# Optimization experiments

Measured on AMD Instinct MI355X. Metric: run time of the kernel, lower is better.

The kernel has to match this reference:

```python
import jax, jax.numpy as jnp
import numpy as np

B, S, D, H, NS = 4, 2048, 1024, 16, 300
DK = D // H                      # 64
NSP = (NS + H - 1) // H * H      # 304 (padded skills)
DG = NSP // H                    # 19
NEG_FILL = -1e9                  # fp32 path in the torch module


def setup_inputs() -> dict:
    key = jax.random.key(0)
    ks = jax.random.split(key, 12)
    sc = 0.02
    return {
        "context_sequence": jax.random.normal(ks[0], (B, S, D), jnp.float32),
        "value_sequence": jax.random.normal(ks[1], (B, S, NS), jnp.float32),
        "mask": jnp.triu(jnp.ones((S, S), jnp.bool_), k=1),  # causal: True = masked
        # weights stored as [in, out] (math-equivalent to torch's x @ W.T + b)
        "Wq": jax.random.normal(ks[2], (D, D), jnp.float32) * sc,
        "bq": jnp.zeros((D,), jnp.float32),
        "Wk": jax.random.normal(ks[3], (D, D), jnp.float32) * sc,
        "bk": jnp.zeros((D,), jnp.float32),
        "Wv": jax.random.normal(ks[4], (NS, NS), jnp.float32) * sc,
        "bv": jnp.zeros((NS,), jnp.float32),
        "Wg": jax.random.normal(ks[5], (NS, D), jnp.float32) * sc,  # gain_to_context
        "bg": jnp.zeros((D,), jnp.float32),
        "Wo": jax.random.normal(ks[6], (D, D), jnp.float32) * sc,   # output_proj
        "bo": jnp.zeros((D,), jnp.float32),
    }


def reference(context_sequence, value_sequence, mask,
              Wq, bq, Wk, bk, Wv, bv, Wg, bg, Wo, bo):
    b = context_sequence.shape[0]
    orig_dtype = context_sequence.dtype

    # Q, K: [b, H, S, DK]
    Q = (context_sequence @ Wq + bq).reshape(b, -1, H, DK).transpose(0, 2, 1, 3)
    K = (context_sequence @ Wk + bk).reshape(b, -1, H, DK).transpose(0, 2, 1, 3)

    # intrinsic-gain V: project in skill space, zero-pad to NSP, split heads -> [b, H, S, DG]
    V_proj = value_sequence @ Wv + bv
    V_proj = jnp.pad(V_proj, ((0, 0), (0, 0), (0, NSP - NS)))
    V = V_proj.reshape(b, -1, H, DG).transpose(0, 2, 1, 3)

    # fp32 score upcast, scale by sqrt(d_k), mask, cast back, softmax
    scores = jnp.einsum('bhqd,bhkd->bhqk',
                        Q.astype(jnp.float32), K.astype(jnp.float32)) / np.sqrt(DK)
    scores = jnp.where(mask, NEG_FILL, scores).astype(orig_dtype)
    attn = jax.nn.softmax(scores, axis=-1)

    # [b, H, S, DG] -> [b, S, NSP] -> slice to NS
    head_gains = jnp.einsum('bhqk,bhkd->bhqd', attn, V)
    agg = head_gains.transpose(0, 2, 1, 3).reshape(b, -1, NSP)[..., :NS]

    output = agg @ Wg + bg            # gain_to_context
    return output @ Wo + bo           # output_proj (dropout is identity in eval)
```

## Files before the change

kernel.cpp:

```cpp
#include <hip/hip_runtime.h>
#include <hip/hip_bf16.h>

#define MROWS 8192
#define DMODEL 1024
#define SLEN 2048
#define NHEADS 16
#define DKH 64
#define DGH 19
#define NSKILL 300
#define KGPAD 320
#define AGG_LD 320
#define QK_LD 2048
#define VK 320
#define VTN 384

typedef __attribute__((ext_vector_type(8))) short short8;
typedef __attribute__((ext_vector_type(4))) float floatx4;

__device__ __forceinline__ float bf2f(unsigned short u) {
  union { unsigned int i; float f; } cv;
  cv.i = ((unsigned int)u) << 16;
  return cv.f;
}
__device__ __forceinline__ unsigned short f2bf(float f) {
  __hip_bfloat16 h = __float2bfloat16(f);
  unsigned short u;
  __builtin_memcpy(&u, &h, 2);
  return u;
}

__device__ __forceinline__ float exp2hw(float x) {
#if __has_builtin(__builtin_amdgcn_exp2f)
  return __builtin_amdgcn_exp2f(x);
#else
  return __expf(x * 0.6931471805599453f);
#endif
}
__device__ __forceinline__ unsigned int cvt_pk_bf16(float lo, float hi) {
  unsigned int r;
  asm("v_cvt_pk_bf16_f32 %0, %1, %2" : "=v"(r) : "v"(lo), "v"(hi));
  return r;
}

__device__ __forceinline__ void ld8(const float* p, float* v) {
  float4 a = *(const float4*)p;
  float4 b = *((const float4*)p + 1);
  v[0]=a.x; v[1]=a.y; v[2]=a.z; v[3]=a.w;
  v[4]=b.x; v[5]=b.y; v[6]=b.z; v[7]=b.w;
}
__device__ __forceinline__ void st1(float* p, float v) { *p = v; }
__device__ __forceinline__ void st1(__hip_bfloat16* p, float v) {
  unsigned short raw = f2bf(v); __builtin_memcpy(p, &raw, 2);
}
__device__ __forceinline__ void st8(__hip_bfloat16* p, const float* v) {
  ushort4 a, b;
  a.x=f2bf(v[0]); a.y=f2bf(v[1]); a.z=f2bf(v[2]); a.w=f2bf(v[3]);
  b.x=f2bf(v[4]); b.y=f2bf(v[5]); b.z=f2bf(v[6]); b.w=f2bf(v[7]);
  *(ushort4*)p = a;
  *((ushort4*)p + 1) = b;
}

__device__ __forceinline__ void gl_lds16(const void* g, void* l) {
  __builtin_amdgcn_global_load_lds(
      (const __attribute__((address_space(1))) unsigned int*)g,
      (__attribute__((address_space(3))) unsigned int*)l, 16, 0, 0);
}

__global__ __launch_bounds__(256)
void prep_mega_kernel(const float* __restrict__ X,
                      const float* __restrict__ Vin,
                      const float* __restrict__ Wg,
                      const float* __restrict__ bq, const float* __restrict__ bk,
                      const float* __restrict__ bv,
                      const float* __restrict__ Wq, const float* __restrict__ Wk,
                      const float* __restrict__ Wo, const float* __restrict__ Wv,
                      __hip_bfloat16* __restrict__ Xb,
                      __hip_bfloat16* __restrict__ Vb16,
                      __hip_bfloat16* __restrict__ Wgb,
                      float* __restrict__ biasqk, float* __restrict__ biasv,
                      float* __restrict__ z384,
                      __hip_bfloat16* __restrict__ Wtqk,
                      __hip_bfloat16* __restrict__ WoT,
                      __hip_bfloat16* __restrict__ Wvt)
{
  const int bid = blockIdx.x;
  const int t = threadIdx.x;
  if (bid < 8192) {
    int i = (bid * 256 + t) * 4;
    float4 v = *(const float4*)(X + i);
    ushort4 s;
    s.x = f2bf(v.x); s.y = f2bf(v.y); s.z = f2bf(v.z); s.w = f2bf(v.w);
    *(ushort4*)((__hip_bfloat16*)Xb + i) = s;
    return;
  }
  if (bid < 9472) {
    int idx = (bid - 8192) * 256 + t;
    int row = idx / 40;
    int c8  = (idx - row * 40) * 8;
    const float* ip = Vin + (size_t)row * NSKILL + c8;
    float v[8];
    if (c8 + 8 <= NSKILL) {
      ld8(ip, v);
    } else {
      #pragma unroll
      for (int u = 0; u < 8; u++)
        v[u] = (c8 + u < NSKILL) ? ip[u] : 0.f;
    }
    st8(Vb16 + (size_t)row * VK + c8, v);
    return;
  }
  if (bid < 9856) {
    int i4 = ((bid - 9472) * 256 + t) * 4;
    int r = i4 >> 10;
    ushort4 s = {0, 0, 0, 0};
    if (r < NSKILL) {
      float4 v = *(const float4*)(Wg + i4);
      s.x = f2bf(v.x); s.y = f2bf(v.y); s.z = f2bf(v.z); s.w = f2bf(v.w);
    }
    *(ushort4*)((__hip_bfloat16*)Wgb + i4) = s;
    return;
  }
  if (bid == 9856) {
    for (int i = t; i < 1024; i += 256) { biasqk[i] = bq[i]; biasqk[1024 + i] = bk[i]; }
    for (int i = t; i < 384; i += 256) {
      biasv[i] = (i < NSKILL) ? bv[i] : 0.f;
      z384[i] = 0.f;
    }
    return;
  }
  const float* W; __hip_bfloat16* Wt; int K, Nld, Ntrue, Kpad, kx, ny;
  if (bid < 10881)      { int l = bid - 9857;  W=Wq; Wt=Wtqk;            K=1024; Nld=1024; Ntrue=1024; Kpad=1024; kx=l&31; ny=l>>5; }
  else if (bid < 11905) { int l = bid - 10881; W=Wk; Wt=Wtqk+1024*1024;  K=1024; Nld=1024; Ntrue=1024; Kpad=1024; kx=l&31; ny=l>>5; }
  else if (bid < 12929) { int l = bid - 11905; W=Wo; Wt=WoT;             K=1024; Nld=1024; Ntrue=1024; Kpad=1024; kx=l&31; ny=l>>5; }
  else                  { int l = bid - 12929; W=Wv; Wt=Wvt;             K=NSKILL; Nld=NSKILL; Ntrue=NSKILL; Kpad=VK; kx=l%10; ny=l/10; }
  __shared__ float tb[32][33];
  const int k0 = kx * 32;
  const int n0 = ny * 32;
  const int tx = t & 31, ty = t >> 5;
  #pragma unroll
  for (int i = 0; i < 4; i++) {
    int k = k0 + ty + i*8;
    int nn = n0 + tx;
    tb[ty + i*8][tx] = (k < K && nn < Ntrue) ? W[(size_t)k * Nld + nn] : 0.f;
  }
  __syncthreads();
  #pragma unroll
  for (int i = 0; i < 4; i++) {
    int nn = n0 + ty + i*8;
    int kk = k0 + tx;
    st1(Wt + (size_t)nn * Kpad + kk, tb[tx][ty + i*8]);
  }
}

__device__ __forceinline__ void gemm_core(const short* __restrict__ Ag,
                                          const short* __restrict__ Bg,
                                          int lda, int ldb, int K,
                                          int m0, int n0,
                                          short* Al, short* Bl,
                                          int tid, floatx4 (&acc)[4][4])
{
  const int lane = tid & 63;
  const int wave = tid >> 6;
  const int wy = wave >> 1, wx = wave & 1;
  const int n = lane & 15;
  const int quad = lane >> 4;

  for (int k0 = 0; k0 < K; k0 += 64) {
    #pragma unroll
    for (int it = 0; it < 4; it++) {
      int ci = it*256 + tid;
      int r = ci >> 3, c = ci & 7;
      int cs = c ^ (r & 7);
      gl_lds16(Ag + (size_t)(m0 + r) * lda + k0 + cs*8, &Al[ci*8]);
    }
    #pragma unroll
    for (int it = 0; it < 4; it++) {
      int ci = it*256 + tid;
      int r = ci >> 3, c = ci & 7;
      int cs = c ^ (r & 7);
      gl_lds16(Bg + (size_t)(n0 + r) * ldb + k0 + cs*8, &Bl[ci*8]);
    }
    __syncthreads();

    #pragma unroll
    for (int s = 0; s < 2; s++) {
      short8 af[4], bfr[4];
      const int c = s*4 + quad;
      #pragma unroll
      for (int i = 0; i < 4; i++) {
        int r = wy*64 + i*16 + n;
        af[i] = *(const short8*)&Al[(r*8 + (c ^ (r & 7)))*8];
      }
      #pragma unroll
      for (int j = 0; j < 4; j++) {
        int r = wx*64 + j*16 + n;
        bfr[j] = *(const short8*)&Bl[(r*8 + (c ^ (r & 7)))*8];
      }
      #pragma unroll
      for (int i = 0; i < 4; i++)
        #pragma unroll
        for (int j = 0; j < 4; j++)
          acc[i][j] = __builtin_amdgcn_mfma_f32_16x16x32_bf16(af[i], bfr[j], acc[i][j], 0, 0, 0);
    }
    __syncthreads();
  }
}

__global__ __launch_bounds__(256)
void gemm_qk_vt_kernel(const __hip_bfloat16* __restrict__ Xb,
                       const __hip_bfloat16* __restrict__ Wtqk,
                       const float* __restrict__ biasqk,
                       __hip_bfloat16* __restrict__ QKbuf,
                       const __hip_bfloat16* __restrict__ Vb16,
                       const __hip_bfloat16* __restrict__ Wvt,
                       const float* __restrict__ biasv,
                       __hip_bfloat16* __restrict__ VT)
{
  __shared__ __align__(16) short Al[128*64];
  __shared__ __align__(16) short Bl[128*64];
  const int tid = threadIdx.x;
  const int lane = tid & 63;
  const int wave = tid >> 6;
  const int wy = wave >> 1, wx = wave & 1;
  const int n = lane & 15;
  const int quad = lane >> 4;

  floatx4 acc[4][4];
  #pragma unroll
  for (int i = 0; i < 4; i++)
    #pragma unroll
    for (int j = 0; j < 4; j++) acc[i][j] = (floatx4){0.f,0.f,0.f,0.f};

  if (blockIdx.x < 1024) {
    const int bx = blockIdx.x & 15, by = blockIdx.x >> 4;
    const int m0 = by * 128, n0 = bx * 128;
    gemm_core((const short*)Xb, (const short*)Wtqk, DMODEL, DMODEL, DMODEL,
              m0, n0, Al, Bl, tid, acc);
    float bj[4];
    #pragma unroll
    for (int j = 0; j < 4; j++) bj[j] = biasqk[n0 + wx*64 + j*16 + n];
    #pragma unroll
    for (int i = 0; i < 4; i++) {
      #pragma unroll
      for (int r = 0; r < 4; r++) {
        int row = m0 + wy*64 + i*16 + quad*4 + r;
        __hip_bfloat16* cp = QKbuf + (size_t)row * QK_LD;
        #pragma unroll
        for (int j = 0; j < 4; j++) {
          int col = n0 + wx*64 + j*16 + n;
          st1(cp + col, acc[i][j][r] + bj[j]);
        }
      }
    }
  } else {
    const int l = blockIdx.x - 1024;
    const int bx = l % 3, by = l / 3;
    const int m0 = by * 128, n0 = bx * 128;
    gemm_core((const short*)Vb16, (const short*)Wvt, VK, VK, VK,
              m0, n0, Al, Bl, tid, acc);
    float bj[4];
    #pragma unroll
    for (int j = 0; j < 4; j++) bj[j] = biasv[n0 + wx*64 + j*16 + n];
    #pragma unroll
    for (int i = 0; i < 4; i++) {
      int row0 = m0 + wy*64 + i*16 + quad*4;
      int bb = row0 >> 11, rin = row0 & 2047;
      #pragma unroll
      for (int j = 0; j < 4; j++) {
        int col = n0 + wx*64 + j*16 + n;
        ushort4 pk;
        pk.x = f2bf(acc[i][j][0] + bj[j]);
        pk.y = f2bf(acc[i][j][1] + bj[j]);
        pk.z = f2bf(acc[i][j][2] + bj[j]);
        pk.w = f2bf(acc[i][j][3] + bj[j]);
        *(ushort4*)(VT + ((size_t)bb * VTN + col) * SLEN + rin) = pk;
      }
    }
  }
}

__global__ __launch_bounds__(256)
void wgo_bgo_kernel(const __hip_bfloat16* __restrict__ WoT,
                    const __hip_bfloat16* __restrict__ Wgb,
                    const float* __restrict__ z384,
                    __hip_bfloat16* __restrict__ WgoT,
                    const float* __restrict__ bg, const float* __restrict__ Wo,
                    const float* __restrict__ bo, float* __restrict__ bgo)
{
  __shared__ __align__(16) short Al[128*64];
  __shared__ __align__(16) short Bl[128*64];
  const int tid = threadIdx.x;
  if (blockIdx.x < 24) {
    const int lane = tid & 63;
    const int wave = tid >> 6;
    const int wy = wave >> 1, wx = wave & 1;
    const int n = lane & 15;
    const int quad = lane >> 4;
    const int bx = blockIdx.x % 3, by = blockIdx.x / 3;
    const int m0 = by * 128, n0 = bx * 128;
    floatx4 acc[4][4];
    #pragma unroll
    for (int i = 0; i < 4; i++)
      #pragma unroll
      for (int j = 0; j < 4; j++) acc[i][j] = (floatx4){0.f,0.f,0.f,0.f};
    gemm_core((const short*)WoT, (const short*)Wgb, DMODEL, DMODEL, DMODEL,
              m0, n0, Al, Bl, tid, acc);
    float bj[4];
    #pragma unroll
    for (int j = 0; j < 4; j++) bj[j] = z384[n0 + wx*64 + j*16 + n];
    #pragma unroll
    for (int i = 0; i < 4; i++) {
      #pragma unroll
      for (int r = 0; r < 4; r++) {
        int row = m0 + wy*64 + i*16 + quad*4 + r;
        __hip_bfloat16* cp = WgoT + (size_t)row * 384;
        #pragma unroll
        for (int j = 0; j < 4; j++) {
          int col = n0 + wx*64 + j*16 + n;
          st1(cp + col, acc[i][j][r] + bj[j]);
        }
      }
    }
  } else {
    __shared__ float red[256];
    const int c   = tid & 15;
    const int jg  = tid >> 4;
    const int col = (blockIdx.x - 24) * 16 + c;
    float acc = 0.f;
    const int j0 = jg * 64;
    #pragma unroll 8
    for (int j = j0; j < j0 + 64; j++)
      acc = fmaf(bg[j], Wo[(size_t)j * DMODEL + col], acc);
    red[tid] = acc;
    __syncthreads();
    if (jg == 0) {
      float s = 0.f;
      #pragma unroll
      for (int g = 0; g < 16; g++) s += red[g*16 + c];
      bgo[col] = s + bo[col];
    }
  }
}

__global__ __launch_bounds__(256)
void gemm_final_kernel(const __hip_bfloat16* __restrict__ A,
                       const __hip_bfloat16* __restrict__ Bt,
                       const float* __restrict__ bias,
                       float* __restrict__ C)
{
  __shared__ __align__(16) short Al[128*64];
  __shared__ __align__(16) short Bl[128*64];
  const int tid = threadIdx.x;
  const int lane = tid & 63;
  const int wave = tid >> 6;
  const int wy = wave >> 1, wx = wave & 1;
  const int n = lane & 15;
  const int quad = lane >> 4;
  const int m0 = blockIdx.y * 128;
  const int n0 = blockIdx.x * 128;
  floatx4 acc[4][4];
  #pragma unroll
  for (int i = 0; i < 4; i++)
    #pragma unroll
    for (int j = 0; j < 4; j++) acc[i][j] = (floatx4){0.f,0.f,0.f,0.f};
  gemm_core((const short*)A, (const short*)Bt, KGPAD, 384, KGPAD,
            m0, n0, Al, Bl, tid, acc);
  float bj[4];
  #pragma unroll
  for (int j = 0; j < 4; j++) bj[j] = bias[n0 + wx*64 + j*16 + n];
  #pragma unroll
  for (int i = 0; i < 4; i++) {
    #pragma unroll
    for (int r = 0; r < 4; r++) {
      int row = m0 + wy*64 + i*16 + quad*4 + r;
      float* cp = C + (size_t)row * DMODEL;
      #pragma unroll
      for (int j = 0; j < 4; j++) {
        int col = n0 + wx*64 + j*16 + n;
        cp[col] = acc[i][j][r] + bj[j];
      }
    }
  }
}

#define ATT_BM 128
#define ATT_BK 64
#define ATT_GRID (24*64)

__global__ __launch_bounds__(256)
void attn_mfma_kernel(const __hip_bfloat16* __restrict__ Qb,
                      const __hip_bfloat16* __restrict__ Kb,
                      const __hip_bfloat16* __restrict__ VTg,
                      __hip_bfloat16* __restrict__ Agg,
                      float* __restrict__ Pl,
                      float* __restrict__ Po)
{
  __shared__ __align__(16) short Kf[2][64*64];
  __shared__ __align__(16) short Vf[2][32*64];
  __shared__ __align__(16) unsigned int Plds[4][2][4][16][4];

  const int tid  = threadIdx.x;
  const int lane = tid & 63;
  const int wave = tid >> 6;
  const int n    = lane & 15;
  const int quad = lane >> 4;

  const int cid = blockIdx.x >> 6;
  const int bh  = blockIdx.x & 63;
  const int h   = bh & 15;
  const int b   = bh >> 4;
  int qt, kt0, nt, mode;
  if (cid == 0)      { qt = 7;       kt0 = 0;  nt = 16; mode = 0; }
  else if (cid <= 8) { qt = cid + 7; kt0 = 0;  nt = 16; mode = 1; }
  else if (cid == 9) { qt = 15;      kt0 = 16; nt = 16; mode = 2; }
  else {
    int e = (cid - 10) >> 1;
    if (((cid - 10) & 1) == 0) { qt = 6 - e;  kt0 = 0;  nt = 14 - 2*e; mode = 0; }
    else                       { qt = 14 - e; kt0 = 16; nt = 14 - 2*e; mode = 2; }
  }
  const int qbase = qt * ATT_BM;
  const size_t bS = (size_t)b * SLEN;

  const float QSCALE = 0.18033688f;
  short8 qf[2][2];
  #pragma unroll
  for (int rf = 0; rf < 2; rf++)
    #pragma unroll
    for (int ks = 0; ks < 2; ks++) {
      const __hip_bfloat16* qp = Qb + (bS + qbase + wave*32 + rf*16 + n) * QK_LD
                                    + h*DKH + ks*32 + quad*8;
      short8 v = *(const short8*)qp;
      #pragma unroll
      for (int e = 0; e < 8; e++) {
        float f = bf2f((unsigned short)v[e]) * QSCALE;
        v[e] = (short)f2bf(f);
      }
      qf[rf][ks] = v;
    }

  const short* kp;
  {
    int f = tid;
    int nn = f & 15, q = (f >> 4) & 3, c = (f >> 6) & 3;
    kp = (const short*)Kb + (bS + kt0*64 + c*16 + nn) * QK_LD + h*DKH + q*8;
  }
  const short* vp;
  {
    int g = tid;
    int vn = g & 15, vq = (g >> 4) & 3, sv = (g >> 6) & 1, cv = g >> 7;
    vp = (const short*)VTg + ((size_t)b * VTN + h*DGH + cv*16 + vn) * SLEN
         + kt0*64 + sv*32 + vq*8;
  }

  floatx4 of[2][2];
  float lrow[2];
  #pragma unroll
  for (int rf = 0; rf < 2; rf++) {
    #pragma unroll
    for (int cv = 0; cv < 2; cv++) of[rf][cv] = (floatx4){0.f,0.f,0.f,0.f};
    lrow[rf] = 0.f;
  }

  const int wrow_max = qbase + wave*32 + 31;

  auto stage = [&](int buf) {
    gl_lds16(kp,      &Kf[buf][tid*8]);
    gl_lds16(kp + 32, &Kf[buf][(tid + 256)*8]);
    gl_lds16(vp,      &Vf[buf][tid*8]);
    kp += 64 * QK_LD;
    vp += 64;
  };

  auto compute_tile = [&](int buf, int kbase) {
    if (kbase > wrow_max) return;
    #pragma unroll
    for (int rf = 0; rf < 2; rf++) {
      floatx4 sf[4];
      __builtin_amdgcn_s_setprio(1);
      #pragma unroll
      for (int cf = 0; cf < 4; cf++) {
        short8 k0v = *(const short8*)&Kf[buf][((0*4 + cf)*64 + lane)*8];
        short8 k1v = *(const short8*)&Kf[buf][((1*4 + cf)*64 + lane)*8];
        floatx4 a2 = (floatx4){0.f,0.f,0.f,0.f};
        a2 = __builtin_amdgcn_mfma_f32_16x16x32_bf16(k0v, qf[rf][0], a2, 0, 0, 0);
        a2 = __builtin_amdgcn_mfma_f32_16x16x32_bf16(k1v, qf[rf][1], a2, 0, 0, 0);
        sf[cf] = a2;
      }
      __builtin_amdgcn_s_setprio(0);

      const int qrow = qbase + wave*32 + rf*16 + n;
      if (kbase + 63 > qbase + wave*32 + rf*16) {
        #pragma unroll
        for (int cf = 0; cf < 4; cf++)
          #pragma unroll
          for (int r = 0; r < 4; r++) {
            int key = kbase + cf*16 + quad*4 + r;
            if (key > qrow) sf[cf][r] = -INFINITY;
          }
      }
      float rs = 0.f;
      #pragma unroll
      for (int cf = 0; cf < 4; cf++)
        #pragma unroll
        for (int r = 0; r < 4; r++) {
          float p = exp2hw(sf[cf][r]);
          sf[cf][r] = p;
          rs += p;
        }
      lrow[rf] += rs;

      #pragma unroll
      for (int cf = 0; cf < 4; cf++) {
        unsigned int w0 = cvt_pk_bf16(sf[cf][0], sf[cf][1]);
        unsigned int w1 = cvt_pk_bf16(sf[cf][2], sf[cf][3]);
        int s   = cf >> 1;
        int qt2 = 2*(cf & 1) + (quad >> 1);
        int jp  = 2*(quad & 1);
        *(uint2*)&Plds[wave][s][qt2][n][jp] = make_uint2(w0, w1);
      }
      short8 p0 = *(const short8*)&Plds[wave][0][quad][n][0];
      short8 p1 = *(const short8*)&Plds[wave][1][quad][n][0];
      __builtin_amdgcn_s_setprio(1);
      #pragma unroll
      for (int cv = 0; cv < 2; cv++) {
        short8 v0 = *(const short8*)&Vf[buf][((cv*2 + 0)*64 + lane)*8];
        short8 v1 = *(const short8*)&Vf[buf][((cv*2 + 1)*64 + lane)*8];
        floatx4 a2 = of[rf][cv];
        a2 = __builtin_amdgcn_mfma_f32_16x16x32_bf16(v0, p0, a2, 0, 0, 0);
        a2 = __builtin_amdgcn_mfma_f32_16x16x32_bf16(v1, p1, a2, 0, 0, 0);
        of[rf][cv] = a2;
      }
      __builtin_amdgcn_s_setprio(0);
    }
  };

  stage(0);
  for (int kt = 0; kt < nt; kt += 2) {
    stage(1);
    asm volatile("s_waitcnt vmcnt(3)" ::: "memory");
    __builtin_amdgcn_s_barrier();
    __builtin_amdgcn_sched_barrier(0);
    compute_tile(0, (kt0 + kt) * ATT_BK);
    __builtin_amdgcn_sched_barrier(0);
    __builtin_amdgcn_s_barrier();

    if (kt + 2 < nt) {
      stage(0);
      asm volatile("s_waitcnt vmcnt(3)" ::: "memory");
    } else {
      asm volatile("s_waitcnt vmcnt(0)" ::: "memory");
    }
    __builtin_amdgcn_s_barrier();
    __builtin_amdgcn_sched_barrier(0);
    compute_tile(1, (kt0 + kt + 1) * ATT_BK);
    __builtin_amdgcn_sched_barrier(0);
    __builtin_amdgcn_s_barrier();
  }

  #pragma unroll
  for (int rf = 0; rf < 2; rf++) {
    lrow[rf] += __shfl_xor(lrow[rf], 16);
    lrow[rf] += __shfl_xor(lrow[rf], 32);
  }

  if (mode == 0) {
    #pragma unroll
    for (int rf = 0; rf < 2; rf++) {
      float inv = 1.f / lrow[rf];
      int row = qbase + wave*32 + rf*16 + n;
      __hip_bfloat16* op = Agg + (bS + row)*AGG_LD + h*DGH;
      #pragma unroll
      for (int cv = 0; cv < 2; cv++)
        #pragma unroll
        for (int r = 0; r < 4; r++) {
          int dim = cv*16 + quad*4 + r;
          if (dim < DGH) st1(op + dim, of[rf][cv][r] * inv);
        }
    }
    if (h == 15) {
      int row = qbase + (tid >> 1);
      int c0 = 304 + (tid & 1) * 8;
      float z[8] = {0.f,0.f,0.f,0.f,0.f,0.f,0.f,0.f};
      st8(Agg + (bS + row)*AGG_LD + c0, z);
    }
  } else {
    const int p = (qt - 8) * 64 + bh;
    const int sl = mode - 1;
    #pragma unroll
    for (int rf = 0; rf < 2; rf++) {
      int rowl = wave*32 + rf*16 + n;
      size_t ri = (size_t)(sl*512 + p)*128 + rowl;
      float* po = Po + ri*20;
      #pragma unroll
      for (int cv = 0; cv < 2; cv++)
        #pragma unroll
        for (int r = 0; r < 4; r++) {
          int dim = cv*16 + quad*4 + r;
          if (dim < DGH) po[dim] = of[rf][cv][r];
        }
      if (quad == 0) Pl[ri] = lrow[rf];
    }
  }
}

__global__ __launch_bounds__(256)
void attn_combine_kernel(const float* __restrict__ Pl,
                         const float* __restrict__ Po,
                         __hip_bfloat16* __restrict__ Agg)
{
  int idx = blockIdx.x * 256 + threadIdx.x;
  int p = idx >> 7, rowl = idx & 127;
  int qt = 8 + (p >> 6), bh = p & 63, h = bh & 15, b = bh >> 4;
  size_t riA = (size_t)p*128 + rowl;
  size_t riB = (size_t)(512 + p)*128 + rowl;
  float inv = 1.f / (Pl[riA] + Pl[riB]);
  const float* oA = Po + riA*20;
  const float* oB = Po + riB*20;
  size_t row = (size_t)b*SLEN + qt*128 + rowl;
  __hip_bfloat16* op = Agg + row*AGG_LD + h*DGH;
  #pragma unroll
  for (int d = 0; d < DGH; d++)
    st1(op + d, (oA[d] + oB[d]) * inv);
  if (h == 15) {
    uint4 z = {0,0,0,0};
    *(uint4*)(Agg + row*AGG_LD + 304) = z;
    *(uint4*)(Agg + row*AGG_LD + 312) = z;
  }
}

extern "C" void kernel_launch(void* const* d_in, const int* in_sizes, int n_in,
                              void* d_out, int out_size, void* d_ws, size_t ws_size,
                              hipStream_t stream) {
  const float* X   = (const float*)d_in[0];
  const float* Vin = (const float*)d_in[1];
  const float* Wq  = (const float*)d_in[3];
  const float* bq  = (const float*)d_in[4];
  const float* Wk  = (const float*)d_in[5];
  const float* bk  = (const float*)d_in[6];
  const float* Wv  = (const float*)d_in[7];
  const float* bv  = (const float*)d_in[8];
  const float* Wg  = (const float*)d_in[9];
  const float* bg  = (const float*)d_in[10];
  const float* Wo  = (const float*)d_in[11];
  const float* bo  = (const float*)d_in[12];
  float* out = (float*)d_out;

  char* ws = (char*)d_ws;
  __hip_bfloat16* Xb    = (__hip_bfloat16*)(ws);
  __hip_bfloat16* AggB  = (__hip_bfloat16*)(ws);
  __hip_bfloat16* WgoT  = (__hip_bfloat16*)(ws + 12582912);
  float*          bgoW  = (float*)         (ws + 13369344);
  __hip_bfloat16* QKbuf = (__hip_bfloat16*)(ws + 16777216);
  __hip_bfloat16* WoT   = (__hip_bfloat16*)(ws + 50331648);

  char* ob = (char*)d_out;
  __hip_bfloat16* Wtqk   = (__hip_bfloat16*)(ob);
  float*          biasqk = (float*)(ob + 4194304);
  __hip_bfloat16* Vb16   = (__hip_bfloat16*)(ob + 4202496);
  float*          biasv  = (float*)(ob + 9445376);
  float*          z384   = (float*)(ob + 9446912);
  __hip_bfloat16* Wgb    = (__hip_bfloat16*)(ob + 9448448);
  __hip_bfloat16* Wvt    = (__hip_bfloat16*)(ob + 10234880);
  float*          Pl     = (float*)(ob + 524288);
  float*          Po     = (float*)(ob + 1048576);
  __hip_bfloat16* VT     = (__hip_bfloat16*)(ob + 12582912);

  dim3 blk(256);
  prep_mega_kernel<<<dim3(13049), blk, 0, stream>>>(
      X, Vin, Wg, bq, bk, bv, Wq, Wk, Wo, Wv,
      Xb, Vb16, Wgb, biasqk, biasv, z384, Wtqk, WoT, Wvt);

  gemm_qk_vt_kernel<<<dim3(1216), blk, 0, stream>>>(
      Xb, Wtqk, biasqk, QKbuf, Vb16, Wvt, biasv, VT);

  wgo_bgo_kernel<<<dim3(88), blk, 0, stream>>>(
      WoT, Wgb, z384, WgoT, bg, Wo, bo, bgoW);

  attn_mfma_kernel<<<dim3(ATT_GRID), dim3(256), 0, stream>>>(
      QKbuf, QKbuf + 1024, VT, AggB, Pl, Po);

  attn_combine_kernel<<<dim3(256), blk, 0, stream>>>(Pl, Po, AggB);

  gemm_final_kernel<<<dim3(8, 64), blk, 0, stream>>>(AggB, WgoT, bgoW, out);
}
```

Before: 267.3 us.

## Merge weight-fold kernel into prep and QK GEMM launches; simplify attention staging

Removes the separate wgo_bgo kernel launch. The bias-fold dot product moves into extra blocks of the prep kernel, and the Wo·Wg fold GEMM moves into extra blocks of the QK/VT GEMM kernel, saving one launch and its tail. Separately, the attention loop drops its double-buffered prefetch with vmcnt waits and raw barriers. It now loads both 64-key tiles at once, then uses __syncthreads before and after computing them. That simplifies synchronization but loses the overlap of global-to-LDS loads with MFMA compute, which could slow the attention kernel.

```diff
diff --git a/kernel.cpp b/kernel.cpp
--- a/kernel.cpp
+++ b/kernel.cpp
@@ -74,6 +74,7 @@
                       const float* __restrict__ bv,
                       const float* __restrict__ Wq, const float* __restrict__ Wk,
                       const float* __restrict__ Wo, const float* __restrict__ Wv,
+                      const float* __restrict__ bg, const float* __restrict__ bo,
                       __hip_bfloat16* __restrict__ Xb,
                       __hip_bfloat16* __restrict__ Vb16,
                       __hip_bfloat16* __restrict__ Wgb,
@@ -81,7 +82,8 @@
                       float* __restrict__ z384,
                       __hip_bfloat16* __restrict__ Wtqk,
                       __hip_bfloat16* __restrict__ WoT,
-                      __hip_bfloat16* __restrict__ Wvt)
+                      __hip_bfloat16* __restrict__ Wvt,
+                      float* __restrict__ bgo)
 {
   const int bid = blockIdx.x;
   const int t = threadIdx.x;
@@ -125,6 +127,26 @@
     for (int i = t; i < 384; i += 256) {
       biasv[i] = (i < NSKILL) ? bv[i] : 0.f;
       z384[i] = 0.f;
+    }
+    return;
+  }
+  if (bid >= 13049) {
+    __shared__ float red[256];
+    const int c   = t & 15;
+    const int jg  = t >> 4;
+    const int col = (bid - 13049) * 16 + c;
+    float acc = 0.f;
+    const int j0 = jg * 64;
+    #pragma unroll 8
+    for (int j = j0; j < j0 + 64; j++)
+      acc = fmaf(bg[j], Wo[(size_t)j * DMODEL + col], acc);
+    red[t] = acc;
+    __syncthreads();
+    if (jg == 0) {
+      float s = 0.f;
+      #pragma unroll
+      for (int g = 0; g < 16; g++) s += red[g*16 + c];
+      bgo[col] = s + bo[col];
     }
     return;
   }
@@ -214,7 +236,11 @@
                        const __hip_bfloat16* __restrict__ Vb16,
                        const __hip_bfloat16* __restrict__ Wvt,
                        const float* __restrict__ biasv,
-                       __hip_bfloat16* __restrict__ VT)
+                       __hip_bfloat16* __restrict__ VT,
+                       const __hip_bfloat16* __restrict__ WoT,
+                       const __hip_bfloat16* __restrict__ Wgb,
+                       const float* __restrict__ z384,
+                       __hip_bfloat16* __restrict__ WgoT)
 {
   __shared__ __align__(16) short Al[128*64];
   __shared__ __align__(16) short Bl[128*64];
@@ -252,7 +278,7 @@
         }
       }
     }
-  } else {
+  } else if (blockIdx.x < 1216) {
     const int l = blockIdx.x - 1024;
     const int bx = l % 3, by = l / 3;
     const int m0 = by * 128, n0 = bx * 128;
@@ -276,33 +302,10 @@
         *(ushort4*)(VT + ((size_t)bb * VTN + col) * SLEN + rin) = pk;
       }
     }
-  }
-}
-
-__global__ __launch_bounds__(256)
-void wgo_bgo_kernel(const __hip_bfloat16* __restrict__ WoT,
-                    const __hip_bfloat16* __restrict__ Wgb,
-                    const float* __restrict__ z384,
-                    __hip_bfloat16* __restrict__ WgoT,
-                    const float* __restrict__ bg, const float* __restrict__ Wo,
-                    const float* __restrict__ bo, float* __restrict__ bgo)
-{
-  __shared__ __align__(16) short Al[128*64];
-  __shared__ __align__(16) short Bl[128*64];
-  const int tid = threadIdx.x;
-  if (blockIdx.x < 24) {
-    const int lane = tid & 63;
-    const int wave = tid >> 6;
-    const int wy = wave >> 1, wx = wave & 1;
-    const int n = lane & 15;
-    const int quad = lane >> 4;
-    const int bx = blockIdx.x % 3, by = blockIdx.x / 3;
+  } else {
+    const int l = blockIdx.x - 1216;
+    const int bx = l % 3, by = l / 3;
     const int m0 = by * 128, n0 = bx * 128;
-    floatx4 acc[4][4];
-    #pragma unroll
-    for (int i = 0; i < 4; i++)
-      #pragma unroll
-      for (int j = 0; j < 4; j++) acc[i][j] = (floatx4){0.f,0.f,0.f,0.f};
     gemm_core((const short*)WoT, (const short*)Wgb, DMODEL, DMODEL, DMODEL,
               m0, n0, Al, Bl, tid, acc);
     float bj[4];
@@ -320,24 +323,6 @@
           st1(cp + col, acc[i][j][r] + bj[j]);
         }
       }
-    }
-  } else {
-    __shared__ float red[256];
-    const int c   = tid & 15;
-    const int jg  = tid >> 4;
-    const int col = (blockIdx.x - 24) * 16 + c;
-    float acc = 0.f;
-    const int j0 = jg * 64;
-    #pragma unroll 8
-    for (int j = j0; j < j0 + 64; j++)
-      acc = fmaf(bg[j], Wo[(size_t)j * DMODEL + col], acc);
-    red[tid] = acc;
-    __syncthreads();
-    if (jg == 0) {
-      float s = 0.f;
-      #pragma unroll
-      for (int g = 0; g < 16; g++) s += red[g*16 + c];
-      bgo[col] = s + bo[col];
     }
   }
 }
@@ -463,12 +448,15 @@
 
   const int wrow_max = qbase + wave*32 + 31;
 
-  auto stage = [&](int buf) {
-    gl_lds16(kp,      &Kf[buf][tid*8]);
-    gl_lds16(kp + 32, &Kf[buf][(tid + 256)*8]);
-    gl_lds16(vp,      &Vf[buf][tid*8]);
-    kp += 64 * QK_LD;
-    vp += 64;
+  auto stage128 = [&]() {
+    gl_lds16(kp,                  &Kf[0][tid*8]);
+    gl_lds16(kp + 32,             &Kf[0][(tid + 256)*8]);
+    gl_lds16(kp + 64*QK_LD,       &Kf[1][tid*8]);
+    gl_lds16(kp + 64*QK_LD + 32,  &Kf[1][(tid + 256)*8]);
+    gl_lds16(vp,                  &Vf[0][tid*8]);
+    gl_lds16(vp + 64,             &Vf[1][tid*8]);
+    kp += 128 * QK_LD;
+    vp += 128;
   };
 
   auto compute_tile = [&](int buf, int kbase) {
@@ -534,27 +522,12 @@
     }
   };
 
-  stage(0);
   for (int kt = 0; kt < nt; kt += 2) {
-    stage(1);
-    asm volatile("s_waitcnt vmcnt(3)" ::: "memory");
-    __builtin_amdgcn_s_barrier();
-    __builtin_amdgcn_sched_barrier(0);
+    stage128();
+    __syncthreads();
     compute_tile(0, (kt0 + kt) * ATT_BK);
-    __builtin_amdgcn_sched_barrier(0);
-    __builtin_amdgcn_s_barrier();
-
-    if (kt + 2 < nt) {
-      stage(0);
-      asm volatile("s_waitcnt vmcnt(3)" ::: "memory");
-    } else {
-      asm volatile("s_waitcnt vmcnt(0)" ::: "memory");
-    }
-    __builtin_amdgcn_s_barrier();
-    __builtin_amdgcn_sched_barrier(0);
     compute_tile(1, (kt0 + kt + 1) * ATT_BK);
-    __builtin_amdgcn_sched_barrier(0);
-    __builtin_amdgcn_s_barrier();
+    __syncthreads();
   }
 
   #pragma unroll
@@ -666,15 +639,12 @@
   __hip_bfloat16* VT     = (__hip_bfloat16*)(ob + 12582912);
 
   dim3 blk(256);
-  prep_mega_kernel<<<dim3(13049), blk, 0, stream>>>(
-      X, Vin, Wg, bq, bk, bv, Wq, Wk, Wo, Wv,
-      Xb, Vb16, Wgb, biasqk, biasv, z384, Wtqk, WoT, Wvt);
-
-  gemm_qk_vt_kernel<<<dim3(1216), blk, 0, stream>>>(
-      Xb, Wtqk, biasqk, QKbuf, Vb16, Wvt, biasv, VT);
-
-  wgo_bgo_kernel<<<dim3(88), blk, 0, stream>>>(
-      WoT, Wgb, z384, WgoT, bg, Wo, bo, bgoW);
+  prep_mega_kernel<<<dim3(13113), blk, 0, stream>>>(
+      X, Vin, Wg, bq, bk, bv, Wq, Wk, Wo, Wv, bg, bo,
+      Xb, Vb16, Wgb, biasqk, biasv, z384, Wtqk, WoT, Wvt, bgoW);
+
+  gemm_qk_vt_kernel<<<dim3(1240), blk, 0, stream>>>(
+      Xb, Wtqk, biasqk, QKbuf, Vb16, Wvt, biasv, VT, WoT, Wgb, z384, WgoT);
 
   attn_mfma_kernel<<<dim3(ATT_GRID), dim3(256), 0, stream>>>(
       QKbuf, QKbuf + 1024, VT, AggB, Pl, Po);
```

Result: no change. 266.2 us (-0.4%).

## Stage both K/V tiles at once and drop software double-buffer pipelining

Applied to the files above, without the earlier changes.

Replaces the two-stage double-buffered prefetch loop in the attention kernel with one step that loads both 64-key K/V tiles and then computes both. The manual vmcnt waits and sched barriers are replaced with two __syncthreads per 128 keys. This halves the barrier count, but global-to-LDS loads no longer overlap with MFMA compute, so memory latency is exposed on every iteration.

```diff
diff --git a/kernel.cpp b/kernel.cpp
--- a/kernel.cpp
+++ b/kernel.cpp
@@ -463,12 +463,15 @@
 
   const int wrow_max = qbase + wave*32 + 31;
 
-  auto stage = [&](int buf) {
-    gl_lds16(kp,      &Kf[buf][tid*8]);
-    gl_lds16(kp + 32, &Kf[buf][(tid + 256)*8]);
-    gl_lds16(vp,      &Vf[buf][tid*8]);
-    kp += 64 * QK_LD;
-    vp += 64;
+  auto stage128 = [&]() {
+    gl_lds16(kp,                  &Kf[0][tid*8]);
+    gl_lds16(kp + 32,             &Kf[0][(tid + 256)*8]);
+    gl_lds16(kp + 64*QK_LD,       &Kf[1][tid*8]);
+    gl_lds16(kp + 64*QK_LD + 32,  &Kf[1][(tid + 256)*8]);
+    gl_lds16(vp,                  &Vf[0][tid*8]);
+    gl_lds16(vp + 64,             &Vf[1][tid*8]);
+    kp += 128 * QK_LD;
+    vp += 128;
   };
 
   auto compute_tile = [&](int buf, int kbase) {
@@ -534,27 +537,12 @@
     }
   };
 
-  stage(0);
   for (int kt = 0; kt < nt; kt += 2) {
-    stage(1);
-    asm volatile("s_waitcnt vmcnt(3)" ::: "memory");
-    __builtin_amdgcn_s_barrier();
-    __builtin_amdgcn_sched_barrier(0);
+    stage128();
+    __syncthreads();
     compute_tile(0, (kt0 + kt) * ATT_BK);
-    __builtin_amdgcn_sched_barrier(0);
-    __builtin_amdgcn_s_barrier();
-
-    if (kt + 2 < nt) {
-      stage(0);
-      asm volatile("s_waitcnt vmcnt(3)" ::: "memory");
-    } else {
-      asm volatile("s_waitcnt vmcnt(0)" ::: "memory");
-    }
-    __builtin_amdgcn_s_barrier();
-    __builtin_amdgcn_sched_barrier(0);
     compute_tile(1, (kt0 + kt + 1) * ATT_BK);
-    __builtin_amdgcn_sched_barrier(0);
-    __builtin_amdgcn_s_barrier();
+    __syncthreads();
   }
 
   #pragma unroll
```

New measurement: 267.8 us. Within noise of the previous version (+0.2%).
